# Kernel tuning notes

Hardware: AMD Instinct MI355X
Metric: run time of the kernel (lower is better)

The kernel has to match this reference:

```python
import jax, jax.numpy as jnp
import numpy as np

B, N, D = 8, 4096, 512


def setup_inputs() -> dict:
    key = jax.random.key(0)
    k1, k2 = jax.random.split(key)
    tgt = jax.random.normal(k1, (B, N, D), dtype=jnp.float32)
    query_pos = jax.random.normal(k2, (B, N, D), dtype=jnp.float32)
    objects_num = N  # scalar int, unused by the math (as in the torch module)
    return {"tgt": tgt, "query_pos": query_pos, "objects_num": objects_num}


def reference(tgt, query_pos, objects_num):
    # L2-normalize along feature dim (torch .norm default: 2-norm, no eps)
    tgt_norm = tgt / jnp.linalg.norm(tgt, axis=-1, keepdims=True)
    # cosine similarity matrix [B, N, N]
    sim = jnp.einsum("bnd,bmd->bnm", tgt_norm, tgt_norm)
    # elementwise tanh, then re-aggregate original (un-normalized) tgt
    out = jnp.einsum("bnm,bmd->bnd", jnp.tanh(sim), tgt)
    return out
```

## Files before the change

kernel.cpp:

```cpp
#include <hip/hip_runtime.h>
#include <hip/hip_bf16.h>

#define B_ 8
#define N_ 4096
#define D_ 512
#define BM 64
#define BK 64
#define NTH 512
#define NT (N_ / BK)

typedef __attribute__((ext_vector_type(8))) short bf16x8;
typedef __attribute__((ext_vector_type(4))) float f32x4;
typedef __attribute__((ext_vector_type(16))) float f32x16;

__device__ __forceinline__ short f2bs(float x) {
  union { __hip_bfloat16 h; short s; } u;
  u.h = __float2bfloat16(x);
  return u.s;
}

__device__ __forceinline__ void gld16(const void* g, void* l) {
  __builtin_amdgcn_global_load_lds((const __attribute__((address_space(1))) void*)g,
                                   (__attribute__((address_space(3))) void*)l, 16, 0, 0);
}

__global__ void __launch_bounds__(256) prep_kernel(const float* __restrict__ tgt,
                                                   ushort* __restrict__ Tbf2,
                                                   ushort* __restrict__ Vt2) {
  __shared__ ushort L[32][520];
  const int id = blockIdx.x;
  const int b = id >> 7, rg = id & 127;
  const int n0 = rg * 32;
  const int t = threadIdx.x;
  const int r = t >> 3, q = t & 7;

  const float* src = tgt + ((size_t)b * N_ + n0 + r) * D_;
  ushort* T2 = Tbf2 + (size_t)b * N_ * D_;
  ushort* V2 = Vt2  + (size_t)b * N_ * D_;

  float4 f[8][2];
  float ss = 0.0f;
  #pragma unroll
  for (int c = 0; c < 8; ++c) {
    const float* p = src + (c * 8 + q) * 8;
    f[c][0] = *(const float4*)p;
    f[c][1] = *(const float4*)(p + 4);
    ss += f[c][0].x * f[c][0].x + f[c][0].y * f[c][0].y
        + f[c][0].z * f[c][0].z + f[c][0].w * f[c][0].w
        + f[c][1].x * f[c][1].x + f[c][1].y * f[c][1].y
        + f[c][1].z * f[c][1].z + f[c][1].w * f[c][1].w;
  }
  ss += __shfl_xor(ss, 1, 64);
  ss += __shfl_xor(ss, 2, 64);
  ss += __shfl_xor(ss, 4, 64);
  const float rs = rsqrtf(ss);

  #pragma unroll
  for (int c = 0; c < 8; ++c) {
    const int g2 = c * 8 + q;
    bf16x8 nv, rv;
    nv[0]=f2bs(f[c][0].x*rs); nv[1]=f2bs(f[c][0].y*rs);
    nv[2]=f2bs(f[c][0].z*rs); nv[3]=f2bs(f[c][0].w*rs);
    nv[4]=f2bs(f[c][1].x*rs); nv[5]=f2bs(f[c][1].y*rs);
    nv[6]=f2bs(f[c][1].z*rs); nv[7]=f2bs(f[c][1].w*rs);
    *(bf16x8*)(T2 + ((size_t)g2 * N_ + n0 + r) * 8) = nv;
    rv[0]=f2bs(f[c][0].x); rv[1]=f2bs(f[c][0].y);
    rv[2]=f2bs(f[c][0].z); rv[3]=f2bs(f[c][0].w);
    rv[4]=f2bs(f[c][1].x); rv[5]=f2bs(f[c][1].y);
    rv[6]=f2bs(f[c][1].z); rv[7]=f2bs(f[c][1].w);
    #pragma unroll
    for (int e = 0; e < 8; ++e) L[r][g2 * 8 + e] = (ushort)rv[e];
  }
  __syncthreads();

  #pragma unroll
  for (int c2 = 0; c2 < 8; ++c2) {
    int tau = c2 * 256 + t;
    int ng = tau >> 9, d = tau & 511;
    bf16x8 v;
    #pragma unroll
    for (int j = 0; j < 8; ++j) v[j] = (short)L[ng * 8 + j][d];
    *(bf16x8*)(V2 + ((size_t)(n0 / 8 + ng) * D_ + d) * 8) = v;
  }
}

__global__ void __launch_bounds__(NTH, 2) fused_kernel(const ushort* __restrict__ Tbf2,
                                                       const ushort* __restrict__ Vt2,
                                                       float* __restrict__ out) {
  __shared__ __align__(16) ushort KV[BK * D_];
  __shared__ __align__(16) ushort VT[BK * D_];
  __shared__ __align__(16) ushort Pl[BM * BK];

  const int id = blockIdx.x;
  const int b  = id & 7;
  const int q0 = (id >> 3) * BM;

  const int lane = threadIdx.x & 63;
  const int w    = threadIdx.x >> 6;

  const ushort* Tb2 = Tbf2 + (size_t)b * N_ * D_;
  const ushort* Vb2 = Vt2  + (size_t)b * N_ * D_;

  const int qG = w >> 1;
  const int mG = w & 1;

  bf16x8 qf[16];
  {
    const int row = q0 + qG * 16 + (lane & 15);
    #pragma unroll
    for (int kk = 0; kk < 16; ++kk) {
      int g = kk * 4 + (lane >> 4);
      qf[kk] = *(const bf16x8*)(Tb2 + ((size_t)g * N_ + row) * 8);
    }
  }

  f32x16 acc[2][2] = {};

  const ushort* kvrd = &KV[(lane >> 4) * 512 + (mG * 32 + (lane & 15)) * 8];
  const ushort* pard = &Pl[(lane >> 5) * 512 + (lane & 31) * 8];
  const ushort* vbrd = &VT[(lane >> 5) * 4096 + (w * 64 + (lane & 31)) * 8];
  ushort*       plwr = &Pl[((mG * 32 + (lane & 15)) >> 3) * 512
                           + (qG * 16 + (lane >> 4) * 4) * 8
                           + ((lane & 15) & 7)];

  const ushort* kvsrc = Tb2 + (size_t)(w * 8) * N_ * 8 + (size_t)BK * 8 + lane * 8;
  const ushort* vtsrc = Vb2 + (size_t)(8 + w) * D_ * 8 + lane * 8;

  #pragma unroll
  for (int i = 0; i < 8; ++i)
    gld16(Tb2 + ((size_t)(w * 8 + i) * N_) * 8 + lane * 8, &KV[(w * 8 + i) * 512]);
  #pragma unroll
  for (int i = 0; i < 8; ++i)
    gld16(Vb2 + (size_t)w * D_ * 8 + i * 512 + lane * 8, &VT[w * 4096 + i * 512]);
  __syncthreads();

  for (int t = 0; t < NT; ++t) {
    f32x4 sacc[2] = {};
    __builtin_amdgcn_s_setprio(1);
    #pragma unroll
    for (int kk = 0; kk < 16; ++kk) {
      bf16x8 b0 = *(const bf16x8*)(kvrd + kk * 2048);
      bf16x8 b1 = *(const bf16x8*)(kvrd + kk * 2048 + 128);
      sacc[0] = __builtin_amdgcn_mfma_f32_16x16x32_bf16(qf[kk], b0, sacc[0], 0, 0, 0);
      sacc[1] = __builtin_amdgcn_mfma_f32_16x16x32_bf16(qf[kk], b1, sacc[1], 0, 0, 0);
    }
    __builtin_amdgcn_s_setprio(0);

    #pragma unroll
    for (int f = 0; f < 2; ++f)
      #pragma unroll
      for (int j = 0; j < 4; ++j) {
        float e = __builtin_amdgcn_exp2f(sacc[f][j] * 2.885390082f);
        float tn = 1.0f - 2.0f * __builtin_amdgcn_rcpf(e + 1.0f);
        plwr[f * 1024 + j * 8] = (ushort)f2bs(tn);
      }
    __syncthreads();

    if (t < NT - 1) {
      #pragma unroll
      for (int i = 0; i < 8; ++i)
        gld16(kvsrc + (size_t)i * N_ * 8, &KV[(w * 8 + i) * 512]);
      kvsrc += BK * 8;
    }

    __builtin_amdgcn_s_setprio(1);
    #pragma unroll
    for (int ks = 0; ks < 4; ++ks) {
      bf16x8 pa0 = *(const bf16x8*)(pard + ks * 1024);
      bf16x8 pa1 = *(const bf16x8*)(pard + ks * 1024 + 256);
      bf16x8 vb0 = *(const bf16x8*)(vbrd + ks * 8192);
      bf16x8 vb1 = *(const bf16x8*)(vbrd + ks * 8192 + 256);
      acc[0][0] = __builtin_amdgcn_mfma_f32_32x32x16_bf16(pa0, vb0, acc[0][0], 0, 0, 0);
      acc[0][1] = __builtin_amdgcn_mfma_f32_32x32x16_bf16(pa0, vb1, acc[0][1], 0, 0, 0);
      acc[1][0] = __builtin_amdgcn_mfma_f32_32x32x16_bf16(pa1, vb0, acc[1][0], 0, 0, 0);
      acc[1][1] = __builtin_amdgcn_mfma_f32_32x32x16_bf16(pa1, vb1, acc[1][1], 0, 0, 0);
    }
    __builtin_amdgcn_s_setprio(0);
    __syncthreads();

    if (t < NT - 1) {
      #pragma unroll
      for (int i = 0; i < 8; ++i)
        gld16(vtsrc + i * 512, &VT[w * 4096 + i * 512]);
      vtsrc += 8 * D_ * 8;
    }
  }

  {
    float* op = out + (size_t)b * N_ * D_ + (size_t)q0 * D_;
    #pragma unroll
    for (int qs = 0; qs < 2; ++qs)
      #pragma unroll
      for (int ds = 0; ds < 2; ++ds) {
        int d = w * 64 + ds * 32 + (lane & 31);
        #pragma unroll
        for (int reg = 0; reg < 16; ++reg) {
          int row = qs * 32 + (reg & 3) + 8 * (reg >> 2) + 4 * (lane >> 5);
          op[(size_t)row * D_ + d] = acc[qs][ds][reg];
        }
      }
  }
}

extern "C" void kernel_launch(void* const* d_in, const int* in_sizes, int n_in,
                              void* d_out, int out_size, void* d_ws, size_t ws_size,
                              hipStream_t stream) {
  const float* tgt = (const float*)d_in[0];
  float* outp = (float*)d_out;

  ushort* Tbf2 = (ushort*)d_ws;
  ushort* Vt2  = Tbf2 + (size_t)B_ * N_ * D_;

  prep_kernel<<<dim3(B_ * 128), dim3(256), 0, stream>>>(tgt, Tbf2, Vt2);
  fused_kernel<<<dim3(B_ * (N_ / BM)), dim3(NTH), 0, stream>>>(Tbf2, Vt2, outp);
}
```

Before: 339.1 us.

## Halve query/key tiles, split QK^T reduction across waves, raise occupancy

Shrinks the query tile and key tile from 64 to 32 and raises launch bounds to four blocks per CU. The QK^T dot product over D is split across two wave groups, and partial sums are combined through an fp32 LDS buffer before tanh. The KV/VT staging is restructured so V loads are issued at the start of each iteration. The goal is better latency hiding through higher occupancy and lower register and LDS use. The costs are a doubled number of K/V tile loads per query row (no reuse across 64 queries), an extra barrier and LDS round trip per iteration, and idle lanes during the tanh step.

After: 455.4 us. 34.3% more time.

```diff
diff --git a/kernel.cpp b/kernel.cpp
--- a/kernel.cpp
+++ b/kernel.cpp
@@ -4,8 +4,8 @@
 #define B_ 8
 #define N_ 4096
 #define D_ 512
-#define BM 64
-#define BK 64
+#define BM 32
+#define BK 32
 #define NTH 512
 #define NT (N_ / BK)
 
@@ -84,12 +84,13 @@
   }
 }
 
-__global__ void __launch_bounds__(NTH, 2) fused_kernel(const ushort* __restrict__ Tbf2,
+__global__ void __launch_bounds__(NTH, 4) fused_kernel(const ushort* __restrict__ Tbf2,
                                                        const ushort* __restrict__ Vt2,
                                                        float* __restrict__ out) {
-  __shared__ __align__(16) ushort KV[BK * D_];
-  __shared__ __align__(16) ushort VT[BK * D_];
-  __shared__ __align__(16) ushort Pl[BM * BK];
+  __shared__ __align__(16) ushort KV[64 * BK * 8];
+  __shared__ __align__(16) ushort VT[4 * D_ * 8];
+  __shared__ float P32[32 * 33];
+  __shared__ __align__(16) ushort Pl[4 * BM * 8];
 
   const int id = blockIdx.x;
   const int b  = id & 7;
@@ -97,108 +98,104 @@
 
   const int lane = threadIdx.x & 63;
   const int w    = threadIdx.x >> 6;
+  const int ks = w & 1, mg = (w >> 1) & 1, qg = w >> 2;
 
   const ushort* Tb2 = Tbf2 + (size_t)b * N_ * D_;
   const ushort* Vb2 = Vt2  + (size_t)b * N_ * D_;
 
-  const int qG = w >> 1;
-  const int mG = w & 1;
-
-  bf16x8 qf[16];
+  bf16x8 qf[8];
   {
-    const int row = q0 + qG * 16 + (lane & 15);
-    #pragma unroll
-    for (int kk = 0; kk < 16; ++kk) {
-      int g = kk * 4 + (lane >> 4);
+    const int row = q0 + qg * 16 + (lane & 15);
+    #pragma unroll
+    for (int kk = 0; kk < 8; ++kk) {
+      int g = ks * 32 + kk * 4 + (lane >> 4);
       qf[kk] = *(const bf16x8*)(Tb2 + ((size_t)g * N_ + row) * 8);
     }
   }
 
-  f32x16 acc[2][2] = {};
-
-  const ushort* kvrd = &KV[(lane >> 4) * 512 + (mG * 32 + (lane & 15)) * 8];
-  const ushort* pard = &Pl[(lane >> 5) * 512 + (lane & 31) * 8];
+  f32x16 acc[2] = {};
+
+  const ushort* kvrd = &KV[(ks * 32 + (lane >> 4)) * 256 + (mg * 16 + (lane & 15)) * 8];
+  const ushort* pard = &Pl[(lane >> 5) * 256 + (lane & 31) * 8];
   const ushort* vbrd = &VT[(lane >> 5) * 4096 + (w * 64 + (lane & 31)) * 8];
-  ushort*       plwr = &Pl[((mG * 32 + (lane & 15)) >> 3) * 512
-                           + (qG * 16 + (lane >> 4) * 4) * 8
-                           + ((lane & 15) & 7)];
-
-  const ushort* kvsrc = Tb2 + (size_t)(w * 8) * N_ * 8 + (size_t)BK * 8 + lane * 8;
-  const ushort* vtsrc = Vb2 + (size_t)(8 + w) * D_ * 8 + lane * 8;
-
-  #pragma unroll
-  for (int i = 0; i < 8; ++i)
-    gld16(Tb2 + ((size_t)(w * 8 + i) * N_) * 8 + lane * 8, &KV[(w * 8 + i) * 512]);
-  #pragma unroll
-  for (int i = 0; i < 8; ++i)
-    gld16(Vb2 + (size_t)w * D_ * 8 + i * 512 + lane * 8, &VT[w * 4096 + i * 512]);
+  const int qbase = qg * 16 + (lane >> 4) * 4;
+  const int mloc  = mg * 16 + (lane & 15);
+  float*  p32p = &P32[qbase * 33 + mloc];
+  ushort* plwr = &Pl[(mloc >> 3) * 256 + qbase * 8 + (mloc & 7)];
+
+  auto STAGE_KV = [&](int mt) {
+    #pragma unroll
+    for (int i = 0; i < 4; ++i) {
+      int c = w * 4 + i;
+      gld16(Tb2 + ((size_t)(2 * c + (lane >> 5)) * N_ + mt * BK + (lane & 31)) * 8,
+            &KV[c * 512]);
+    }
+  };
+  auto STAGE_VT = [&](int mt) {
+    #pragma unroll
+    for (int i = 0; i < 4; ++i) {
+      int c = w * 4 + i;
+      gld16(Vb2 + ((size_t)(mt * 4 + (c >> 3)) * D_ + (c & 7) * 64 + lane) * 8,
+            &VT[(c >> 3) * 4096 + (c & 7) * 512]);
+    }
+  };
+
+  STAGE_KV(0);
+  STAGE_VT(0);
   __syncthreads();
 
   for (int t = 0; t < NT; ++t) {
-    f32x4 sacc[2] = {};
+    if (t >= 1) STAGE_VT(t);
+    f32x4 sacc = {};
     __builtin_amdgcn_s_setprio(1);
     #pragma unroll
-    for (int kk = 0; kk < 16; ++kk) {
-      bf16x8 b0 = *(const bf16x8*)(kvrd + kk * 2048);
-      bf16x8 b1 = *(const bf16x8*)(kvrd + kk * 2048 + 128);
-      sacc[0] = __builtin_amdgcn_mfma_f32_16x16x32_bf16(qf[kk], b0, sacc[0], 0, 0, 0);
-      sacc[1] = __builtin_amdgcn_mfma_f32_16x16x32_bf16(qf[kk], b1, sacc[1], 0, 0, 0);
+    for (int kk = 0; kk < 8; ++kk) {
+      bf16x8 bf = *(const bf16x8*)(kvrd + kk * 1024);
+      sacc = __builtin_amdgcn_mfma_f32_16x16x32_bf16(qf[kk], bf, sacc, 0, 0, 0);
     }
     __builtin_amdgcn_s_setprio(0);
-
-    #pragma unroll
-    for (int f = 0; f < 2; ++f)
+    if (ks == 1) {
+      #pragma unroll
+      for (int j = 0; j < 4; ++j) p32p[j * 33] = sacc[j];
+    }
+    __syncthreads();
+
+    if (ks == 0) {
       #pragma unroll
       for (int j = 0; j < 4; ++j) {
-        float e = __builtin_amdgcn_exp2f(sacc[f][j] * 2.885390082f);
+        float s = sacc[j] + p32p[j * 33];
+        float e = __builtin_amdgcn_exp2f(s * 2.885390082f);
         float tn = 1.0f - 2.0f * __builtin_amdgcn_rcpf(e + 1.0f);
-        plwr[f * 1024 + j * 8] = (ushort)f2bs(tn);
+        plwr[j * 8] = (ushort)f2bs(tn);
       }
+    }
     __syncthreads();
 
-    if (t < NT - 1) {
-      #pragma unroll
-      for (int i = 0; i < 8; ++i)
-        gld16(kvsrc + (size_t)i * N_ * 8, &KV[(w * 8 + i) * 512]);
-      kvsrc += BK * 8;
-    }
-
+    STAGE_KV((t + 1) & (NT - 1));
     __builtin_amdgcn_s_setprio(1);
     #pragma unroll
-    for (int ks = 0; ks < 4; ++ks) {
-      bf16x8 pa0 = *(const bf16x8*)(pard + ks * 1024);
-      bf16x8 pa1 = *(const bf16x8*)(pard + ks * 1024 + 256);
-      bf16x8 vb0 = *(const bf16x8*)(vbrd + ks * 8192);
-      bf16x8 vb1 = *(const bf16x8*)(vbrd + ks * 8192 + 256);
-      acc[0][0] = __builtin_amdgcn_mfma_f32_32x32x16_bf16(pa0, vb0, acc[0][0], 0, 0, 0);
-      acc[0][1] = __builtin_amdgcn_mfma_f32_32x32x16_bf16(pa0, vb1, acc[0][1], 0, 0, 0);
-      acc[1][0] = __builtin_amdgcn_mfma_f32_32x32x16_bf16(pa1, vb0, acc[1][0], 0, 0, 0);
-      acc[1][1] = __builtin_amdgcn_mfma_f32_32x32x16_bf16(pa1, vb1, acc[1][1], 0, 0, 0);
+    for (int kstep = 0; kstep < 2; ++kstep) {
+      bf16x8 pa = *(const bf16x8*)(pard + kstep * 512);
+      bf16x8 v0 = *(const bf16x8*)(vbrd + kstep * 8192);
+      bf16x8 v1 = *(const bf16x8*)(vbrd + kstep * 8192 + 256);
+      acc[0] = __builtin_amdgcn_mfma_f32_32x32x16_bf16(pa, v0, acc[0], 0, 0, 0);
+      acc[1] = __builtin_amdgcn_mfma_f32_32x32x16_bf16(pa, v1, acc[1], 0, 0, 0);
     }
     __builtin_amdgcn_s_setprio(0);
     __syncthreads();
-
-    if (t < NT - 1) {
-      #pragma unroll
-      for (int i = 0; i < 8; ++i)
-        gld16(vtsrc + i * 512, &VT[w * 4096 + i * 512]);
-      vtsrc += 8 * D_ * 8;
-    }
   }
 
   {
     float* op = out + (size_t)b * N_ * D_ + (size_t)q0 * D_;
     #pragma unroll
-    for (int qs = 0; qs < 2; ++qs)
+    for (int dt = 0; dt < 2; ++dt) {
+      int d = w * 64 + dt * 32 + (lane & 31);
       #pragma unroll
-      for (int ds = 0; ds < 2; ++ds) {
-        int d = w * 64 + ds * 32 + (lane & 31);
-        #pragma unroll
-        for (int reg = 0; reg < 16; ++reg) {
-          int row = qs * 32 + (reg & 3) + 8 * (reg >> 2) + 4 * (lane >> 5);
-          op[(size_t)row * D_ + d] = acc[qs][ds][reg];
-        }
+      for (int reg = 0; reg < 16; ++reg) {
+        int row = (reg & 3) + 8 * (reg >> 2) + 4 * (lane >> 5);
+        op[(size_t)row * D_ + d] = acc[dt][reg];
       }
+    }
   }
 }
 
```

## Double query tile to 128 rows per block to halve K/V streaming

Applied to the files above, without the earlier changes.

Raises the query block from 64 to 128 rows, so each of the 8 waves owns 16 query rows and computes similarity against all 64 keys of the tile. The P@V stage then accumulates four 32-row output blocks per wave. This doubles arithmetic per loaded K/V tile and halves the grid, cutting global and LDS traffic per output. In exchange, accumulator registers double (128 floats for acc), which may hurt occupancy or cause spills under launch_bounds(512,2). The grid also drops to 256 blocks, which may leave some CUs underused.

After: 280.3 us, median of 2. -17.3%, faster.

```diff
diff --git a/kernel.cpp b/kernel.cpp
--- a/kernel.cpp
+++ b/kernel.cpp
@@ -4,7 +4,7 @@
 #define B_ 8
 #define N_ 4096
 #define D_ 512
-#define BM 64
+#define BM 128
 #define BK 64
 #define NTH 512
 #define NT (N_ / BK)
@@ -97,12 +97,10 @@
 
   const int lane = threadIdx.x & 63;
   const int w    = threadIdx.x >> 6;
+  const int qG   = w;
 
   const ushort* Tb2 = Tbf2 + (size_t)b * N_ * D_;
   const ushort* Vb2 = Vt2  + (size_t)b * N_ * D_;
-
-  const int qG = w >> 1;
-  const int mG = w & 1;
 
   bf16x8 qf[16];
   {
@@ -114,14 +112,14 @@
     }
   }
 
-  f32x16 acc[2][2] = {};
-
-  const ushort* kvrd = &KV[(lane >> 4) * 512 + (mG * 32 + (lane & 15)) * 8];
-  const ushort* pard = &Pl[(lane >> 5) * 512 + (lane & 31) * 8];
+  f32x16 acc[4][2] = {};
+
+  const ushort* kvrd = &KV[(lane >> 4) * 512 + (lane & 15) * 8];
+  const ushort* pard = &Pl[(lane >> 5) * 1024 + (lane & 31) * 8];
   const ushort* vbrd = &VT[(lane >> 5) * 4096 + (w * 64 + (lane & 31)) * 8];
-  ushort*       plwr = &Pl[((mG * 32 + (lane & 15)) >> 3) * 512
+  ushort*       plwr = &Pl[((lane & 15) >> 3) * 1024
                            + (qG * 16 + (lane >> 4) * 4) * 8
-                           + ((lane & 15) & 7)];
+                           + (lane & 7)];
 
   const ushort* kvsrc = Tb2 + (size_t)(w * 8) * N_ * 8 + (size_t)BK * 8 + lane * 8;
   const ushort* vtsrc = Vb2 + (size_t)(8 + w) * D_ * 8 + lane * 8;
@@ -135,24 +133,25 @@
   __syncthreads();
 
   for (int t = 0; t < NT; ++t) {
-    f32x4 sacc[2] = {};
+    f32x4 sacc[4] = {};
     __builtin_amdgcn_s_setprio(1);
     #pragma unroll
     for (int kk = 0; kk < 16; ++kk) {
-      bf16x8 b0 = *(const bf16x8*)(kvrd + kk * 2048);
-      bf16x8 b1 = *(const bf16x8*)(kvrd + kk * 2048 + 128);
-      sacc[0] = __builtin_amdgcn_mfma_f32_16x16x32_bf16(qf[kk], b0, sacc[0], 0, 0, 0);
-      sacc[1] = __builtin_amdgcn_mfma_f32_16x16x32_bf16(qf[kk], b1, sacc[1], 0, 0, 0);
+      #pragma unroll
+      for (int f = 0; f < 4; ++f) {
+        bf16x8 bf = *(const bf16x8*)(kvrd + kk * 2048 + f * 128);
+        sacc[f] = __builtin_amdgcn_mfma_f32_16x16x32_bf16(qf[kk], bf, sacc[f], 0, 0, 0);
+      }
     }
     __builtin_amdgcn_s_setprio(0);
 
     #pragma unroll
-    for (int f = 0; f < 2; ++f)
+    for (int f = 0; f < 4; ++f)
       #pragma unroll
       for (int j = 0; j < 4; ++j) {
         float e = __builtin_amdgcn_exp2f(sacc[f][j] * 2.885390082f);
         float tn = 1.0f - 2.0f * __builtin_amdgcn_rcpf(e + 1.0f);
-        plwr[f * 1024 + j * 8] = (ushort)f2bs(tn);
+        plwr[f * 2048 + j * 8] = (ushort)f2bs(tn);
       }
     __syncthreads();
 
@@ -166,14 +165,14 @@
     __builtin_amdgcn_s_setprio(1);
     #pragma unroll
     for (int ks = 0; ks < 4; ++ks) {
-      bf16x8 pa0 = *(const bf16x8*)(pard + ks * 1024);
-      bf16x8 pa1 = *(const bf16x8*)(pard + ks * 1024 + 256);
       bf16x8 vb0 = *(const bf16x8*)(vbrd + ks * 8192);
       bf16x8 vb1 = *(const bf16x8*)(vbrd + ks * 8192 + 256);
-      acc[0][0] = __builtin_amdgcn_mfma_f32_32x32x16_bf16(pa0, vb0, acc[0][0], 0, 0, 0);
-      acc[0][1] = __builtin_amdgcn_mfma_f32_32x32x16_bf16(pa0, vb1, acc[0][1], 0, 0, 0);
-      acc[1][0] = __builtin_amdgcn_mfma_f32_32x32x16_bf16(pa1, vb0, acc[1][0], 0, 0, 0);
-      acc[1][1] = __builtin_amdgcn_mfma_f32_32x32x16_bf16(pa1, vb1, acc[1][1], 0, 0, 0);
+      #pragma unroll
+      for (int qb = 0; qb < 4; ++qb) {
+        bf16x8 pa = *(const bf16x8*)(pard + ks * 2048 + qb * 256);
+        acc[qb][0] = __builtin_amdgcn_mfma_f32_32x32x16_bf16(pa, vb0, acc[qb][0], 0, 0, 0);
+        acc[qb][1] = __builtin_amdgcn_mfma_f32_32x32x16_bf16(pa, vb1, acc[qb][1], 0, 0, 0);
+      }
     }
     __builtin_amdgcn_s_setprio(0);
     __syncthreads();
@@ -189,14 +188,14 @@
   {
     float* op = out + (size_t)b * N_ * D_ + (size_t)q0 * D_;
     #pragma unroll
-    for (int qs = 0; qs < 2; ++qs)
+    for (int qb = 0; qb < 4; ++qb)
       #pragma unroll
       for (int ds = 0; ds < 2; ++ds) {
         int d = w * 64 + ds * 32 + (lane & 31);
         #pragma unroll
         for (int reg = 0; reg < 16; ++reg) {
-          int row = qs * 32 + (reg & 3) + 8 * (reg >> 2) + 4 * (lane >> 5);
-          op[(size_t)row * D_ + d] = acc[qs][ds][reg];
+          int row = qb * 32 + (reg & 3) + 8 * (reg >> 2) + 4 * (lane >> 5);
+          op[(size_t)row * D_ + d] = acc[qb][ds][reg];
         }
       }
   }
```
